# Kernel tuning notes

Hardware: AMD Instinct MI355X
Metric: run time of the kernel (lower is better)

The kernel has to match this reference:

```python
import jax, jax.numpy as jnp
import numpy as np

MARGIN = 1.0
EPS = 1e-12  # safe sqrt/normalize clamp; used entries have magnitude >> EPS


def _normalize(x):
    return x / jnp.maximum(jnp.linalg.norm(x, axis=-1, keepdims=True), EPS)


def _cdist(x, y):
    # Pairwise L2 distances, matches torch.cdist(p=2)
    sq = (jnp.sum(x * x, axis=-1)[:, None]
          + jnp.sum(y * y, axis=-1)[None, :]
          - 2.0 * (x @ y.T))
    return jnp.sqrt(jnp.maximum(sq, EPS))


def setup_inputs() -> dict:
    key = jax.random.key(0)
    k1, k2, k3 = jax.random.split(key, 3)
    B, P, D = 4096, 2, 256
    anchor = jax.random.normal(k1, (B, D), dtype=jnp.float32)
    positive = jax.random.normal(k2, (B, P, D), dtype=jnp.float32)
    labels = jax.random.randint(k3, (B,), 0, 200)
    return {"anchor": anchor, "positive": positive, "labels": labels}


def reference(anchor, positive, labels):
    a = _normalize(anchor)            # [B, D]
    p = _normalize(positive)          # [B, P, D]
    B = a.shape[0]
    all_labels = jnp.concatenate([labels, labels])           # [2B]
    neg_mask = all_labels[None, :] != labels[:, None]        # [B, 2B]
    idx = jnp.arange(B)
    losses = []
    for v in range(p.shape[1]):  # loop over small fixed num_positives
        feats = jnp.concatenate([a, p[:, v]], axis=0)        # [2B, D]
        dist = _cdist(feats, feats)                          # [2B, 2B]
        pos_dist = dist[idx, idx + B]                        # [B]
        # hard negative mining: min distance over different-label columns
        neg_dist = jnp.min(jnp.where(neg_mask, dist[:B], jnp.inf), axis=1)  # [B]
        losses.append(jnp.maximum(pos_dist - neg_dist + MARGIN, 0.0))
    return jnp.mean(jnp.stack(losses))
```

## Files before the change

kernel.cpp:

```cpp
#include <hip/hip_runtime.h>
#include <hip/hip_bf16.h>

#define NB    4096
#define ND    256
#define NP    2
#define TOT   (NB * 3)
#define RB    256
#define NCHUNK 48
#define COLS_PER_CHUNK 256
#define TILES (COLS_PER_CHUNK / 16)
#define NEG_INIT (-4.0f)

typedef float f32x4 __attribute__((ext_vector_type(4)));
typedef long  longx2 __attribute__((ext_vector_type(2)));

#define WS_F_OFF    0
#define WS_POS_OFF  (TOT * RB)
#define WS_PART_OFF (WS_POS_OFF + NB * NP * 4)

__global__ void norm_pos_kernel(const float* __restrict__ anchor,
                                const float* __restrict__ positive,
                                unsigned char* __restrict__ F,
                                float* __restrict__ posArr) {
    int wid = threadIdx.x >> 6, lane = threadIdx.x & 63;
    int row = blockIdx.x * 4 + wid;
    if (row < NB) {
        const float* src = anchor + (size_t)row * ND;
        float4 x = *(const float4*)(src + lane * 4);
        float ss = x.x * x.x + x.y * x.y + x.z * x.z + x.w * x.w;
        #pragma unroll
        for (int m = 1; m < 64; m <<= 1) ss += __shfl_xor(ss, m, 64);
        float inv = 1.0f / fmaxf(sqrtf(ss), 1e-12f);
        int pk = __builtin_amdgcn_cvt_pk_fp8_f32(x.x * inv, x.y * inv, 0, false);
        pk = __builtin_amdgcn_cvt_pk_fp8_f32(x.z * inv, x.w * inv, pk, true);
        *(int*)(F + (size_t)row * RB + lane * 4) = pk;
    } else {
        int q = row - NB;
        int v = q >> 12;
        int j = q & (NB - 1);
        const float* sp = positive + (size_t)(j * NP + v) * ND;
        const float* sa = anchor + (size_t)j * ND;
        float4 xp = *(const float4*)(sp + lane * 4);
        float4 xa = *(const float4*)(sa + lane * 4);
        float sspv = xp.x * xp.x + xp.y * xp.y + xp.z * xp.z + xp.w * xp.w;
        float ssa  = xa.x * xa.x + xa.y * xa.y + xa.z * xa.z + xa.w * xa.w;
        float dot  = xa.x * xp.x + xa.y * xp.y + xa.z * xp.z + xa.w * xp.w;
        #pragma unroll
        for (int m = 1; m < 64; m <<= 1) {
            sspv += __shfl_xor(sspv, m, 64);
            ssa  += __shfl_xor(ssa, m, 64);
            dot  += __shfl_xor(dot, m, 64);
        }
        float invp = 1.0f / fmaxf(sqrtf(sspv), 1e-12f);
        int pk = __builtin_amdgcn_cvt_pk_fp8_f32(xp.x * invp, xp.y * invp, 0, false);
        pk = __builtin_amdgcn_cvt_pk_fp8_f32(xp.z * invp, xp.w * invp, pk, true);
        *(int*)(F + (size_t)row * RB + lane * 4) = pk;
        if (lane == 0) {
            float inva = 1.0f / fmaxf(sqrtf(ssa), 1e-12f);
            float dn = dot * inva * invp;
            float sq = 2.0f - 2.0f * dn;
            posArr[j * NP + v] = sqrtf(fmaxf(sq, 1e-12f));
        }
    }
}

__global__ __launch_bounds__(256, 2) void gram_max_kernel(
        const unsigned char* __restrict__ F,
        const int* __restrict__ labels,
        float* __restrict__ partials) {
    __shared__ unsigned char ldsB[TILES * 4096];
    __shared__ int slab[COLS_PER_CHUNK];
    int tid = threadIdx.x;
    int wid = tid >> 6, lane = tid & 63;
    int l15 = lane & 15, quad = lane >> 4;

    int id = blockIdx.x;
    int chunk = id >> 4;
    int rbi   = id & 15;

    int rowBase = rbi * 256 + wid * 64;
    int col0 = chunk * COLS_PER_CHUNK;
    int part = chunk >> 4;
    const unsigned char* Fb = F;

    long af[4][8];
    #pragma unroll
    for (int s = 0; s < 4; ++s) {
        const unsigned char* ar = Fb + (size_t)(rowBase + s * 16 + l15) * RB + quad * 8;
        #pragma unroll
        for (int kk = 0; kk < 8; ++kk)
            af[s][kk] = *(const long*)(ar + kk * 32);
    }
    unsigned rlp[4];
    #pragma unroll
    for (int s = 0; s < 4; ++s) {
        const int* lb = labels + rowBase + s * 16 + quad * 4;
        rlp[s] = (unsigned)lb[0] | ((unsigned)lb[1] << 8)
               | ((unsigned)lb[2] << 16) | ((unsigned)lb[3] << 24);
    }

    slab[tid] = labels[(col0 & (NB - 1)) + tid];
    {
        const unsigned char* g = Fb + (size_t)(col0 + tid) * RB;
        int tilec = tid >> 4, c15 = tid & 15;
        unsigned char* dbase = ldsB + tilec * 4096 + c15 * 8;
        #pragma unroll
        for (int kk = 0; kk < 8; ++kk) {
            longx2 u = *(const longx2*)(g + kk * 32);
            longx2 v = *(const longx2*)(g + kk * 32 + 16);
            unsigned char* d = dbase + kk * 512;
            *(long*)(d + 0 * 128) = u.x;
            *(long*)(d + 1 * 128) = u.y;
            *(long*)(d + 2 * 128) = v.x;
            *(long*)(d + 3 * 128) = v.y;
        }
    }
    __syncthreads();

    float vmax[4][4];
    #pragma unroll
    for (int s = 0; s < 4; ++s)
        #pragma unroll
        for (int r = 0; r < 4; ++r) vmax[s][r] = NEG_INIT;

    #pragma unroll 2
    for (int ct = 0; ct < TILES; ++ct) {
        long bfr[8];
        #pragma unroll
        for (int kk = 0; kk < 8; ++kk)
            bfr[kk] = *(const long*)&ldsB[ct * 4096 + kk * 512 + lane * 8];

        int lc = slab[ct * 16 + l15];
        unsigned lcq = (unsigned)lc * 0x01010101u;

        f32x4 acc[4];
        #pragma unroll
        for (int s = 0; s < 4; ++s) acc[s] = (f32x4){0.f, 0.f, 0.f, 0.f};
        #pragma unroll
        for (int kk = 0; kk < 8; ++kk)
            #pragma unroll
            for (int s = 0; s < 4; ++s)
                acc[s] = __builtin_amdgcn_mfma_f32_16x16x32_fp8_fp8(af[s][kk], bfr[kk], acc[s], 0, 0, 0);

        #pragma unroll
        for (int s = 0; s < 4; ++s) {
            unsigned x = rlp[s] ^ lcq;
            #pragma unroll
            for (int r = 0; r < 4; ++r) {
                bool neq = ((x >> (8 * r)) & 0xffu) != 0u;
                vmax[s][r] = fmaxf(vmax[s][r], neq ? acc[s][r] : NEG_INIT);
            }
        }
    }

    #pragma unroll
    for (int m = 1; m < 16; m <<= 1)
        #pragma unroll
        for (int s = 0; s < 4; ++s)
            #pragma unroll
            for (int r = 0; r < 4; ++r)
                vmax[s][r] = fmaxf(vmax[s][r], __shfl_xor(vmax[s][r], m, 64));

    if (l15 == 0) {
        #pragma unroll
        for (int s = 0; s < 4; ++s)
            #pragma unroll
            for (int r = 0; r < 4; ++r) {
                int row = rowBase + s * 16 + quad * 4 + r;
                partials[(size_t)part * NB * 16 + (size_t)row * 16 + (chunk & 15)] = vmax[s][r];
            }
    }
}

__global__ void finalize_kernel(const float* __restrict__ partials,
                                const float* __restrict__ posArr,
                                float* __restrict__ out) {
    int row = blockIdx.x * 256 + threadIdx.x;
    const float* pa = partials + (size_t)row * 16;
    const float* pb = pa + (size_t)NB * 16;
    const float* pc = pb + (size_t)NB * 16;
    float ma = NEG_INIT, m0 = NEG_INIT, m1 = NEG_INIT;
    #pragma unroll
    for (int j = 0; j < 16; ++j) {
        ma = fmaxf(ma, pa[j]);
        m0 = fmaxf(m0, pb[j]);
        m1 = fmaxf(m1, pc[j]);
    }
    float n0 = sqrtf(fmaxf(2.0f - 2.0f * fmaxf(ma, m0), 1e-12f));
    float n1 = sqrtf(fmaxf(2.0f - 2.0f * fmaxf(ma, m1), 1e-12f));
    float l = fmaxf(posArr[row * 2 + 0] - n0 + 1.0f, 0.0f)
            + fmaxf(posArr[row * 2 + 1] - n1 + 1.0f, 0.0f);
    int lane = threadIdx.x & 63, wid = threadIdx.x >> 6;
    #pragma unroll
    for (int m = 1; m < 64; m <<= 1) l += __shfl_xor(l, m, 64);
    __shared__ float wsum[4];
    if (lane == 0) wsum[wid] = l;
    __syncthreads();
    if (threadIdx.x == 0) {
        float s = wsum[0] + wsum[1] + wsum[2] + wsum[3];
        atomicAdd(out, s * (1.0f / (NB * NP)));
    }
}

extern "C" void kernel_launch(void* const* d_in, const int* in_sizes, int n_in,
                              void* d_out, int out_size, void* d_ws, size_t ws_size,
                              hipStream_t stream) {
    const float* anchor   = (const float*)d_in[0];
    const float* positive = (const float*)d_in[1];
    const int*   labels   = (const int*)d_in[2];
    float* out = (float*)d_out;

    unsigned char* F = (unsigned char*)((char*)d_ws + WS_F_OFF);
    float* posArr    = (float*)((char*)d_ws + WS_POS_OFF);
    float* partials  = (float*)((char*)d_ws + WS_PART_OFF);

    norm_pos_kernel<<<TOT / 4, 256, 0, stream>>>(anchor, positive, F, posArr);
    gram_max_kernel<<<(NB / 256) * NCHUNK, 256, 0, stream>>>(F, labels, partials);
    hipMemsetAsync(d_out, 0, sizeof(float), stream);
    finalize_kernel<<<NB / 256, 256, 0, stream>>>(partials, posArr, out);
}
```

Before: 95.31 us.

## Halve LDS tile buffer and prefetch second column half during compute

The column-chunk staging is split into two phases of 128 columns, using a 32 KB LDS buffer instead of 64 KB. The second phase's global loads are issued into registers before the first phase's MFMA loop, so they can overlap compute, and are written to LDS between barriers. The smaller LDS footprint and launch bounds raised to 3 blocks per CU aim for higher occupancy. In exchange it adds register pressure from the 16 prefetch registers and extra barriers, which may cause spills under the tighter register budget.

```diff
diff --git a/kernel.cpp b/kernel.cpp
--- a/kernel.cpp
+++ b/kernel.cpp
@@ -8,7 +8,7 @@
 #define RB    256
 #define NCHUNK 48
 #define COLS_PER_CHUNK 256
-#define TILES (COLS_PER_CHUNK / 16)
+#define TILES 16
 #define NEG_INIT (-4.0f)
 
 typedef float f32x4 __attribute__((ext_vector_type(4)));
@@ -64,11 +64,11 @@
     }
 }
 
-__global__ __launch_bounds__(256, 2) void gram_max_kernel(
+__global__ __launch_bounds__(256, 3) void gram_max_kernel(
         const unsigned char* __restrict__ F,
         const int* __restrict__ labels,
         float* __restrict__ partials) {
-    __shared__ unsigned char ldsB[TILES * 4096];
+    __shared__ unsigned char ldsB[8 * 4096];
     __shared__ int slab[COLS_PER_CHUNK];
     int tid = threadIdx.x;
     int wid = tid >> 6, lane = tid & 63;
@@ -83,6 +83,34 @@
     int part = chunk >> 4;
     const unsigned char* Fb = F;
 
+    int cp = tid & 127, h = tid >> 7;
+    int kkb = h * 4;
+    int slot = cp >> 4;
+    int c15 = cp & 15;
+
+    long bt[4][4];
+    auto stage_load = [&](int phase) {
+        const unsigned char* g = Fb + (size_t)(col0 + phase * 128 + cp) * RB + kkb * 32;
+        #pragma unroll
+        for (int j = 0; j < 4; ++j) {
+            longx2 u = *(const longx2*)(g + j * 32);
+            longx2 v = *(const longx2*)(g + j * 32 + 16);
+            bt[j][0] = u.x; bt[j][1] = u.y; bt[j][2] = v.x; bt[j][3] = v.y;
+        }
+    };
+    auto stage_write = [&]() {
+        unsigned char* d = ldsB + slot * 4096 + kkb * 512 + c15 * 8;
+        #pragma unroll
+        for (int j = 0; j < 4; ++j)
+            #pragma unroll
+            for (int q = 0; q < 4; ++q)
+                *(long*)(d + j * 512 + q * 128) = bt[j][q];
+    };
+
+    slab[tid] = labels[(col0 & (NB - 1)) + tid];
+    stage_load(0);
+    stage_write();
+
     long af[4][8];
     #pragma unroll
     for (int s = 0; s < 4; ++s) {
@@ -99,57 +127,51 @@
                | ((unsigned)lb[2] << 16) | ((unsigned)lb[3] << 24);
     }
 
-    slab[tid] = labels[(col0 & (NB - 1)) + tid];
-    {
-        const unsigned char* g = Fb + (size_t)(col0 + tid) * RB;
-        int tilec = tid >> 4, c15 = tid & 15;
-        unsigned char* dbase = ldsB + tilec * 4096 + c15 * 8;
-        #pragma unroll
-        for (int kk = 0; kk < 8; ++kk) {
-            longx2 u = *(const longx2*)(g + kk * 32);
-            longx2 v = *(const longx2*)(g + kk * 32 + 16);
-            unsigned char* d = dbase + kk * 512;
-            *(long*)(d + 0 * 128) = u.x;
-            *(long*)(d + 1 * 128) = u.y;
-            *(long*)(d + 2 * 128) = v.x;
-            *(long*)(d + 3 * 128) = v.y;
-        }
-    }
+    float vmax[4][4];
+    #pragma unroll
+    for (int s = 0; s < 4; ++s)
+        #pragma unroll
+        for (int r = 0; r < 4; ++r) vmax[s][r] = NEG_INIT;
+
     __syncthreads();
-
-    float vmax[4][4];
-    #pragma unroll
-    for (int s = 0; s < 4; ++s)
-        #pragma unroll
-        for (int r = 0; r < 4; ++r) vmax[s][r] = NEG_INIT;
-
-    #pragma unroll 2
-    for (int ct = 0; ct < TILES; ++ct) {
-        long bfr[8];
-        #pragma unroll
-        for (int kk = 0; kk < 8; ++kk)
-            bfr[kk] = *(const long*)&ldsB[ct * 4096 + kk * 512 + lane * 8];
-
-        int lc = slab[ct * 16 + l15];
-        unsigned lcq = (unsigned)lc * 0x01010101u;
-
-        f32x4 acc[4];
-        #pragma unroll
-        for (int s = 0; s < 4; ++s) acc[s] = (f32x4){0.f, 0.f, 0.f, 0.f};
-        #pragma unroll
-        for (int kk = 0; kk < 8; ++kk)
-            #pragma unroll
-            for (int s = 0; s < 4; ++s)
-                acc[s] = __builtin_amdgcn_mfma_f32_16x16x32_fp8_fp8(af[s][kk], bfr[kk], acc[s], 0, 0, 0);
-
-        #pragma unroll
-        for (int s = 0; s < 4; ++s) {
-            unsigned x = rlp[s] ^ lcq;
-            #pragma unroll
-            for (int r = 0; r < 4; ++r) {
-                bool neq = ((x >> (8 * r)) & 0xffu) != 0u;
-                vmax[s][r] = fmaxf(vmax[s][r], neq ? acc[s][r] : NEG_INIT);
+    stage_load(1);
+
+    #pragma unroll
+    for (int phase = 0; phase < 2; ++phase) {
+        int ctBase = phase * 8;
+        for (int t = 0; t < 8; ++t) {
+            int ct = ctBase + t;
+            long bfr[8];
+            #pragma unroll
+            for (int kk = 0; kk < 8; ++kk)
+                bfr[kk] = *(const long*)&ldsB[t * 4096 + kk * 512 + lane * 8];
+
+            int lc = slab[ct * 16 + l15];
+            unsigned lcq = (unsigned)lc * 0x01010101u;
+
+            f32x4 acc[4];
+            #pragma unroll
+            for (int s = 0; s < 4; ++s) acc[s] = (f32x4){0.f, 0.f, 0.f, 0.f};
+            #pragma unroll
+            for (int kk = 0; kk < 8; ++kk)
+                #pragma unroll
+                for (int s = 0; s < 4; ++s)
+                    acc[s] = __builtin_amdgcn_mfma_f32_16x16x32_fp8_fp8(af[s][kk], bfr[kk], acc[s], 0, 0, 0);
+
+            #pragma unroll
+            for (int s = 0; s < 4; ++s) {
+                unsigned x = rlp[s] ^ lcq;
+                #pragma unroll
+                for (int r = 0; r < 4; ++r) {
+                    bool neq = ((x >> (8 * r)) & 0xffu) != 0u;
+                    vmax[s][r] = fmaxf(vmax[s][r], neq ? acc[s][r] : NEG_INIT);
+                }
             }
+        }
+        if (phase == 0) {
+            __syncthreads();
+            stage_write();
+            __syncthreads();
         }
     }
 
```

Measured after the change: 113.2 us. 18.8% more time.

## Store FP8 features pre-swizzled in MFMA tile layout for coalesced loads

Applied to the files above, without the earlier changes.

The normalization kernel now writes FP8 features directly in the 16-row MFMA operand tile layout, grouped in 4KB blocks. The gram kernel can then fill LDS with contiguous float4 copies and load A fragments with coalesced 8-byte strided reads instead of gathering scattered row segments. This removes the transpose/scatter work in the gram kernel's LDS fill. The change also drops the min-blocks-per-CU launch bound hint and moves label staging before the copy. In exchange, the norm kernel's stores become scattered.

```diff
diff --git a/kernel.cpp b/kernel.cpp
--- a/kernel.cpp
+++ b/kernel.cpp
@@ -5,25 +5,27 @@
 #define ND    256
 #define NP    2
 #define TOT   (NB * 3)
-#define RB    256
 #define NCHUNK 48
 #define COLS_PER_CHUNK 256
-#define TILES (COLS_PER_CHUNK / 16)
+#define TILES 16
 #define NEG_INIT (-4.0f)
 
 typedef float f32x4 __attribute__((ext_vector_type(4)));
-typedef long  longx2 __attribute__((ext_vector_type(2)));
 
 #define WS_F_OFF    0
-#define WS_POS_OFF  (TOT * RB)
+#define WS_POS_OFF  (TOT * 256)
 #define WS_PART_OFF (WS_POS_OFF + NB * NP * 4)
 
 __global__ void norm_pos_kernel(const float* __restrict__ anchor,
                                 const float* __restrict__ positive,
-                                unsigned char* __restrict__ F,
+                                unsigned char* __restrict__ F2,
                                 float* __restrict__ posArr) {
     int wid = threadIdx.x >> 6, lane = threadIdx.x & 63;
     int row = blockIdx.x * 4 + wid;
+    int group = row >> 4, r15 = row & 15;
+    int kk = lane >> 3, quad = (lane >> 1) & 3, jj = (lane & 1) * 4;
+    int* dst = (int*)(F2 + (size_t)group * 4096 + kk * 512 + (quad * 16 + r15) * 8 + jj);
+
     if (row < NB) {
         const float* src = anchor + (size_t)row * ND;
         float4 x = *(const float4*)(src + lane * 4);
@@ -33,7 +35,7 @@
         float inv = 1.0f / fmaxf(sqrtf(ss), 1e-12f);
         int pk = __builtin_amdgcn_cvt_pk_fp8_f32(x.x * inv, x.y * inv, 0, false);
         pk = __builtin_amdgcn_cvt_pk_fp8_f32(x.z * inv, x.w * inv, pk, true);
-        *(int*)(F + (size_t)row * RB + lane * 4) = pk;
+        *dst = pk;
     } else {
         int q = row - NB;
         int v = q >> 12;
@@ -54,7 +56,7 @@
         float invp = 1.0f / fmaxf(sqrtf(sspv), 1e-12f);
         int pk = __builtin_amdgcn_cvt_pk_fp8_f32(xp.x * invp, xp.y * invp, 0, false);
         pk = __builtin_amdgcn_cvt_pk_fp8_f32(xp.z * invp, xp.w * invp, pk, true);
-        *(int*)(F + (size_t)row * RB + lane * 4) = pk;
+        *dst = pk;
         if (lane == 0) {
             float inva = 1.0f / fmaxf(sqrtf(ssa), 1e-12f);
             float dn = dot * inva * invp;
@@ -64,8 +66,8 @@
     }
 }
 
-__global__ __launch_bounds__(256, 2) void gram_max_kernel(
-        const unsigned char* __restrict__ F,
+__global__ __launch_bounds__(256) void gram_max_kernel(
+        const unsigned char* __restrict__ F2,
         const int* __restrict__ labels,
         float* __restrict__ partials) {
     __shared__ unsigned char ldsB[TILES * 4096];
@@ -81,15 +83,24 @@
     int rowBase = rbi * 256 + wid * 64;
     int col0 = chunk * COLS_PER_CHUNK;
     int part = chunk >> 4;
-    const unsigned char* Fb = F;
+
+    slab[tid] = labels[(col0 & (NB - 1)) + tid];
+
+    {
+        const float4* src = (const float4*)(F2 + (size_t)chunk * 16 * 4096);
+        float4* dst = (float4*)ldsB;
+        #pragma unroll
+        for (int j = 0; j < 16; ++j)
+            dst[tid + j * 256] = src[tid + j * 256];
+    }
 
     long af[4][8];
     #pragma unroll
     for (int s = 0; s < 4; ++s) {
-        const unsigned char* ar = Fb + (size_t)(rowBase + s * 16 + l15) * RB + quad * 8;
+        const unsigned char* ab = F2 + (size_t)(rbi * 16 + wid * 4 + s) * 4096 + lane * 8;
         #pragma unroll
         for (int kk = 0; kk < 8; ++kk)
-            af[s][kk] = *(const long*)(ar + kk * 32);
+            af[s][kk] = *(const long*)(ab + kk * 512);
     }
     unsigned rlp[4];
     #pragma unroll
@@ -99,29 +110,13 @@
                | ((unsigned)lb[2] << 16) | ((unsigned)lb[3] << 24);
     }
 
-    slab[tid] = labels[(col0 & (NB - 1)) + tid];
-    {
-        const unsigned char* g = Fb + (size_t)(col0 + tid) * RB;
-        int tilec = tid >> 4, c15 = tid & 15;
-        unsigned char* dbase = ldsB + tilec * 4096 + c15 * 8;
-        #pragma unroll
-        for (int kk = 0; kk < 8; ++kk) {
-            longx2 u = *(const longx2*)(g + kk * 32);
-            longx2 v = *(const longx2*)(g + kk * 32 + 16);
-            unsigned char* d = dbase + kk * 512;
-            *(long*)(d + 0 * 128) = u.x;
-            *(long*)(d + 1 * 128) = u.y;
-            *(long*)(d + 2 * 128) = v.x;
-            *(long*)(d + 3 * 128) = v.y;
-        }
-    }
+    float vmax[4][4];
+    #pragma unroll
+    for (int s = 0; s < 4; ++s)
+        #pragma unroll
+        for (int r = 0; r < 4; ++r) vmax[s][r] = NEG_INIT;
+
     __syncthreads();
-
-    float vmax[4][4];
-    #pragma unroll
-    for (int s = 0; s < 4; ++s)
-        #pragma unroll
-        for (int r = 0; r < 4; ++r) vmax[s][r] = NEG_INIT;
 
     #pragma unroll 2
     for (int ct = 0; ct < TILES; ++ct) {
@@ -210,12 +205,12 @@
     const int*   labels   = (const int*)d_in[2];
     float* out = (float*)d_out;
 
-    unsigned char* F = (unsigned char*)((char*)d_ws + WS_F_OFF);
-    float* posArr    = (float*)((char*)d_ws + WS_POS_OFF);
-    float* partials  = (float*)((char*)d_ws + WS_PART_OFF);
-
-    norm_pos_kernel<<<TOT / 4, 256, 0, stream>>>(anchor, positive, F, posArr);
-    gram_max_kernel<<<(NB / 256) * NCHUNK, 256, 0, stream>>>(F, labels, partials);
+    unsigned char* F2 = (unsigned char*)((char*)d_ws + WS_F_OFF);
+    float* posArr     = (float*)((char*)d_ws + WS_POS_OFF);
+    float* partials   = (float*)((char*)d_ws + WS_PART_OFF);
+
+    norm_pos_kernel<<<TOT / 4, 256, 0, stream>>>(anchor, positive, F2, posArr);
+    gram_max_kernel<<<(NB / 256) * NCHUNK, 256, 0, stream>>>(F2, labels, partials);
     hipMemsetAsync(d_out, 0, sizeof(float), stream);
     finalize_kernel<<<NB / 256, 256, 0, stream>>>(partials, posArr, out);
 }
```

Measured after the change: 93.57 us. Within noise of the previous version (-1.8%).
